# Performance work log

Measured on AMD Instinct MI355X. Metric: run time of the kernel, lower is better.

Reference implementation:

```python
import jax, jax.numpy as jnp
import numpy as np
import math

B, S, HID, H = 2, 1024, 768, 12
D = HID // H  # 64
ALPHA = 32.0


def setup_inputs() -> dict:
    key = jax.random.key(0)
    ks = jax.random.split(key, 8)
    return {
        "hidden_states": jax.random.normal(ks[0], (B, S, HID), jnp.float32),
        "attention_mask": jnp.zeros((B, 1, 1, S), jnp.float32),
        "head_mask": jnp.ones((1, H, 1, 1), jnp.float32),
        "rel_pos": jax.random.normal(ks[1], (B, H, S, S), jnp.float32),
        "rel_2d_pos": jax.random.normal(ks[2], (B, H, S, S), jnp.float32),
        "Wq": jax.random.normal(ks[3], (HID, HID), jnp.float32) * 0.02,
        "bq": jnp.zeros((HID,), jnp.float32),
        "Wk": jax.random.normal(ks[4], (HID, HID), jnp.float32) * 0.02,
        "bk": jnp.zeros((HID,), jnp.float32),
        "Wv": jax.random.normal(ks[5], (HID, HID), jnp.float32) * 0.02,
        "bv": jnp.zeros((HID,), jnp.float32),
    }


def _heads(x):
    # [B,S,HID] -> [B,H,S,D]
    return x.reshape(B, S, H, D).transpose(0, 2, 1, 3)


def cogview_softmax(scores, alpha=ALPHA):
    s = scores / alpha
    m = jnp.max(s, axis=-1, keepdims=True)
    return jax.nn.softmax((s - m) * alpha, axis=-1)


def reference(hidden_states, attention_mask, head_mask, rel_pos, rel_2d_pos,
              Wq, bq, Wk, bk, Wv, bv):
    norm = math.sqrt(D)
    q = _heads(hidden_states @ Wq + bq) / norm   # [B,H,S,D]
    k = _heads(hidden_states @ Wk + bk)
    v = _heads(hidden_states @ Wv + bv)
    scores = jnp.einsum("bhsd,bhtd->bhst", q, k)
    scores = scores + (rel_pos + rel_2d_pos) / norm
    scores = scores + attention_mask
    probs = cogview_softmax(scores)              # [B,H,S,S]
    probs = probs * head_mask
    ctx = jnp.einsum("bhst,bhtd->bhsd", probs, v)
    ctx = ctx.transpose(0, 2, 1, 3).reshape(B, S, HID)
    return ctx
```

## Files before the change

### kernel.cpp

```cpp
#include <hip/hip_runtime.h>
#include <hip/hip_bf16.h>
#include <cstdint>

#define BB   2
#define SS   1024
#define HIDD 768
#define NH   12
#define DH   64
#define BH   (BB*NH)

typedef short bf16x8 __attribute__((ext_vector_type(8)));
typedef float f32x4  __attribute__((ext_vector_type(4)));

__device__ __forceinline__ unsigned short f2b(float x) {
    union { float f; uint32_t u; } v; v.f = x;
    uint32_t u = v.u;
    uint32_t r = (u + 0x7fffu + ((u >> 16) & 1u)) >> 16;
    return (unsigned short)r;
}

__device__ __forceinline__ void async16(const void* g, void* l) {
    __builtin_amdgcn_global_load_lds(
        (const __attribute__((address_space(1))) unsigned int*)g,
        (__attribute__((address_space(3))) unsigned int*)l,
        16, 0, 0);
}

__global__ void cvt_x(const float* __restrict__ x, unsigned short* __restrict__ xb) {
    int i = blockIdx.x * blockDim.x + threadIdx.x;
    float4 v = ((const float4*)x)[i];
    ushort4 o;
    o.x = f2b(v.x); o.y = f2b(v.y); o.z = f2b(v.z); o.w = f2b(v.w);
    ((ushort4*)xb)[i] = o;
}

__global__ void transpose_w(const float* __restrict__ Wq, const float* __restrict__ Wk,
                            const float* __restrict__ Wv, unsigned short* __restrict__ Wt) {
    __shared__ float tile[32][33];
    const int w = blockIdx.z;
    const float* W = (w == 0) ? Wq : (w == 1) ? Wk : Wv;
    const int tx = threadIdx.x & 31, ty = threadIdx.x >> 5;
    const int k0 = blockIdx.x * 32, n0 = blockIdx.y * 32;
    for (int p = 0; p < 4; ++p)
        tile[ty + p * 8][tx] = W[(k0 + ty + p * 8) * HIDD + n0 + tx];
    __syncthreads();
    for (int p = 0; p < 4; ++p) {
        int n = n0 + ty + p * 8;
        Wt[(w * HIDD + n) * HIDD + k0 + tx] = f2b(tile[tx][ty + p * 8]);
    }
}

__global__ __launch_bounds__(256) void qkv_gemm(
    const unsigned short* __restrict__ Xb, const unsigned short* __restrict__ Wt,
    const float* __restrict__ bq, const float* __restrict__ bk, const float* __restrict__ bv,
    unsigned short* __restrict__ Qh, unsigned short* __restrict__ Kh,
    unsigned short* __restrict__ VhT) {
    __shared__ __align__(16) unsigned short lA[128 * 32];
    __shared__ __align__(16) unsigned short lB[128 * 32];
    const int t = threadIdx.x;
    const int wave = t >> 6, lane = t & 63;
    const int l15 = lane & 15, quad = lane >> 4;
    const int m0 = blockIdx.x * 128;
    const int n0 = blockIdx.y * 128;
    const int wm = (wave >> 1) * 64, wn = (wave & 1) * 64;

    f32x4 acc[4][4] = {};

    for (int k0 = 0; k0 < HIDD; k0 += 32) {
        __syncthreads();
        for (int r = 0; r < 2; ++r) {
            int i = r * 256 + t;
            int ldsbase = (r * 256 + wave * 64) * 8;
            async16(Xb + (m0 + (i >> 2)) * HIDD + k0 + (i & 3) * 8, &lA[ldsbase]);
            async16(Wt + (n0 + (i >> 2)) * HIDD + k0 + (i & 3) * 8, &lB[ldsbase]);
        }
        __syncthreads();

        bf16x8 af[4], bf[4];
        #pragma unroll
        for (int i = 0; i < 4; ++i)
            af[i] = *(const bf16x8*)&lA[(wm + i * 16 + l15) * 32 + quad * 8];
        #pragma unroll
        for (int j = 0; j < 4; ++j)
            bf[j] = *(const bf16x8*)&lB[(wn + j * 16 + l15) * 32 + quad * 8];
        #pragma unroll
        for (int i = 0; i < 4; ++i)
            #pragma unroll
            for (int j = 0; j < 4; ++j)
                acc[i][j] = __builtin_amdgcn_mfma_f32_16x16x32_bf16(af[i], bf[j], acc[i][j], 0, 0, 0);
    }

    const int sect = (n0 >= 1536) ? 2 : (n0 >= 768) ? 1 : 0;
    const float* bias = (sect == 0) ? bq : (sect == 1) ? bk : bv;
    #pragma unroll
    for (int i = 0; i < 4; ++i) {
        #pragma unroll
        for (int j = 0; j < 4; ++j) {
            int n  = n0 + wn + j * 16 + l15;
            int nn = n - sect * HIDD;
            int h = nn >> 6, d = nn & 63;
            float bval = bias[nn];
            #pragma unroll
            for (int r = 0; r < 4; ++r) {
                int m = m0 + wm + i * 16 + quad * 4 + r;
                int b = m >> 10, s = m & 1023;
                float v = acc[i][j][r] + bval;
                if (sect == 0) {
                    Qh[((size_t)(b * NH + h) * SS + s) * DH + d] = f2b(v * 0.125f);
                } else if (sect == 1) {
                    Kh[((size_t)(b * NH + h) * SS + s) * DH + d] = f2b(v);
                } else {
                    VhT[((size_t)(b * NH + h) * DH + d) * SS + s] = f2b(v);
                }
            }
        }
    }
}

__global__ __launch_bounds__(256) void flash_attn(
    const unsigned short* __restrict__ Qh, const unsigned short* __restrict__ Kh,
    const unsigned short* __restrict__ VhT,
    const float* __restrict__ rel, const float* __restrict__ rel2d,
    const float* __restrict__ amask, const float* __restrict__ hmask,
    float* __restrict__ out) {
    __shared__ __align__(16) unsigned short Plds[4][16 * 72];

    const int t = threadIdx.x;
    const int wave = t >> 6, lane = t & 63;
    const int l15 = lane & 15, quad = lane >> 4;
    const int bh = blockIdx.y;
    const int b = bh / NH, h = bh % NH;
    const int m0 = blockIdx.x * 64 + wave * 16;

    const unsigned short* Qp = Qh + (size_t)bh * SS * DH;
    const unsigned short* Kp = Kh + (size_t)bh * SS * DH;
    const unsigned short* Vp = VhT + (size_t)bh * DH * SS;
    const float* relp  = rel   + (size_t)bh * SS * SS;
    const float* rel2p = rel2d + (size_t)bh * SS * SS;
    const float* maskp = amask + (size_t)b * SS;

    bf16x8 qf0 = *(const bf16x8*)&Qp[(m0 + l15) * DH + quad * 8];
    bf16x8 qf1 = *(const bf16x8*)&Qp[(m0 + l15) * DH + 32 + quad * 8];

    f32x4 o[4] = {};
    float mrow[4] = {-1e30f, -1e30f, -1e30f, -1e30f};
    float lrow[4] = {0.f, 0.f, 0.f, 0.f};
    unsigned short* Pw = &Plds[wave][0];

    for (int j0 = 0; j0 < SS; j0 += 64) {
        f32x4 sc[4] = {};
        #pragma unroll
        for (int c = 0; c < 4; ++c) {
            bf16x8 k0f = *(const bf16x8*)&Kp[(j0 + c * 16 + l15) * DH + quad * 8];
            bf16x8 k1f = *(const bf16x8*)&Kp[(j0 + c * 16 + l15) * DH + 32 + quad * 8];
            sc[c] = __builtin_amdgcn_mfma_f32_16x16x32_bf16(qf0, k0f, sc[c], 0, 0, 0);
            sc[c] = __builtin_amdgcn_mfma_f32_16x16x32_bf16(qf1, k1f, sc[c], 0, 0, 0);
        }
        float sv[4][4];
        #pragma unroll
        for (int c = 0; c < 4; ++c) {
            int col = j0 + c * 16 + l15;
            float mk = maskp[col];
            #pragma unroll
            for (int r = 0; r < 4; ++r) {
                size_t idx = (size_t)(m0 + quad * 4 + r) * SS + col;
                sv[c][r] = sc[c][r] + (relp[idx] + rel2p[idx]) * 0.125f + mk;
            }
        }
        float alpha[4];
        #pragma unroll
        for (int r = 0; r < 4; ++r) {
            float mx = fmaxf(fmaxf(sv[0][r], sv[1][r]), fmaxf(sv[2][r], sv[3][r]));
            #pragma unroll
            for (int off = 1; off < 16; off <<= 1) mx = fmaxf(mx, __shfl_xor(mx, off, 64));
            float mnew = fmaxf(mrow[r], mx);
            alpha[r] = __expf(mrow[r] - mnew);
            mrow[r] = mnew;
            float rs = 0.f;
            #pragma unroll
            for (int c = 0; c < 4; ++c) {
                float p = __expf(sv[c][r] - mnew);
                sv[c][r] = p;
                rs += p;
            }
            #pragma unroll
            for (int off = 1; off < 16; off <<= 1) rs += __shfl_xor(rs, off, 64);
            lrow[r] = lrow[r] * alpha[r] + rs;
            o[0][r] *= alpha[r]; o[1][r] *= alpha[r]; o[2][r] *= alpha[r]; o[3][r] *= alpha[r];
        }
        #pragma unroll
        for (int c = 0; c < 4; ++c)
            #pragma unroll
            for (int r = 0; r < 4; ++r)
                Pw[(quad * 4 + r) * 72 + c * 16 + l15] = f2b(sv[c][r]);

        bf16x8 pf0 = *(const bf16x8*)&Pw[l15 * 72 + quad * 8];
        bf16x8 pf1 = *(const bf16x8*)&Pw[l15 * 72 + 32 + quad * 8];
        #pragma unroll
        for (int dt = 0; dt < 4; ++dt) {
            bf16x8 v0 = *(const bf16x8*)&Vp[(dt * 16 + l15) * SS + j0 + quad * 8];
            bf16x8 v1 = *(const bf16x8*)&Vp[(dt * 16 + l15) * SS + j0 + 32 + quad * 8];
            o[dt] = __builtin_amdgcn_mfma_f32_16x16x32_bf16(pf0, v0, o[dt], 0, 0, 0);
            o[dt] = __builtin_amdgcn_mfma_f32_16x16x32_bf16(pf1, v1, o[dt], 0, 0, 0);
        }
    }

    const float hm = hmask[h];
    #pragma unroll
    for (int r = 0; r < 4; ++r) {
        float inv = hm / lrow[r];
        int s = m0 + quad * 4 + r;
        float* op = out + ((size_t)(b * SS + s)) * HIDD + h * DH;
        #pragma unroll
        for (int dt = 0; dt < 4; ++dt) op[dt * 16 + l15] = o[dt][r] * inv;
    }
}

extern "C" void kernel_launch(void* const* d_in, const int* in_sizes, int n_in,
                              void* d_out, int out_size, void* d_ws, size_t ws_size,
                              hipStream_t stream) {
    const float* hs    = (const float*)d_in[0];
    const float* am    = (const float*)d_in[1];
    const float* hm    = (const float*)d_in[2];
    const float* rel   = (const float*)d_in[3];
    const float* rel2d = (const float*)d_in[4];
    const float* Wq    = (const float*)d_in[5];
    const float* bq    = (const float*)d_in[6];
    const float* Wk    = (const float*)d_in[7];
    const float* bk    = (const float*)d_in[8];
    const float* Wv    = (const float*)d_in[9];
    const float* bv    = (const float*)d_in[10];
    float* out = (float*)d_out;

    unsigned short* Xb  = (unsigned short*)d_ws;
    unsigned short* Wt  = Xb + 2048 * HIDD;
    unsigned short* Qh  = Wt + 3 * HIDD * HIDD;
    unsigned short* Kh  = Qh + (size_t)BH * SS * DH;
    unsigned short* VhT = Kh + (size_t)BH * SS * DH;

    cvt_x<<<(2048 * HIDD / 4) / 256, 256, 0, stream>>>(hs, Xb);
    dim3 gT(24, 24, 3);
    transpose_w<<<gT, 256, 0, stream>>>(Wq, Wk, Wv, Wt);
    dim3 gG(16, 18);
    qkv_gemm<<<gG, 256, 0, stream>>>(Xb, Wt, bq, bk, bv, Qh, Kh, VhT);
    dim3 gF(16, BH);
    flash_attn<<<gF, 256, 0, stream>>>(Qh, Kh, VhT, rel, rel2d, am, hm, out);
}
```

Before: 305.7 us.

## Split attention KV range across waves, shrink GEMM tile, add V transpose

Flash attention now gives each block 16 query rows and has its four waves each process a quarter of the key range, merging partial max/sum/output through shared memory. This quadruples the grid so more blocks are in flight while streaming the large rel_pos tensors. The QKV GEMM uses 64-row tiles, doubling its grid, and writes V in row layout with a coalesced store; a separate transpose kernel then builds V^T. The cost is an extra launch, an extra V round trip through memory, and an LDS reduction step in attention.

```diff
diff --git a/kernel.cpp b/kernel.cpp
--- a/kernel.cpp
+++ b/kernel.cpp
@@ -54,37 +54,40 @@
     const unsigned short* __restrict__ Xb, const unsigned short* __restrict__ Wt,
     const float* __restrict__ bq, const float* __restrict__ bk, const float* __restrict__ bv,
     unsigned short* __restrict__ Qh, unsigned short* __restrict__ Kh,
-    unsigned short* __restrict__ VhT) {
-    __shared__ __align__(16) unsigned short lA[128 * 32];
+    unsigned short* __restrict__ Vh) {
+    __shared__ __align__(16) unsigned short lA[64 * 32];
     __shared__ __align__(16) unsigned short lB[128 * 32];
     const int t = threadIdx.x;
     const int wave = t >> 6, lane = t & 63;
     const int l15 = lane & 15, quad = lane >> 4;
-    const int m0 = blockIdx.x * 128;
+    const int m0 = blockIdx.x * 64;
     const int n0 = blockIdx.y * 128;
-    const int wm = (wave >> 1) * 64, wn = (wave & 1) * 64;
-
-    f32x4 acc[4][4] = {};
+    const int wm = (wave >> 1) * 32, wn = (wave & 1) * 64;
+
+    f32x4 acc[2][4] = {};
 
     for (int k0 = 0; k0 < HIDD; k0 += 32) {
         __syncthreads();
-        for (int r = 0; r < 2; ++r) {
-            int i = r * 256 + t;
-            int ldsbase = (r * 256 + wave * 64) * 8;
-            async16(Xb + (m0 + (i >> 2)) * HIDD + k0 + (i & 3) * 8, &lA[ldsbase]);
-            async16(Wt + (n0 + (i >> 2)) * HIDD + k0 + (i & 3) * 8, &lB[ldsbase]);
+        {
+            int ldsA = (wave * 64) * 8;
+            async16(Xb + (m0 + (t >> 2)) * HIDD + k0 + (t & 3) * 8, &lA[ldsA]);
+            for (int r = 0; r < 2; ++r) {
+                int i = r * 256 + t;
+                int ldsB = (r * 256 + wave * 64) * 8;
+                async16(Wt + (n0 + (i >> 2)) * HIDD + k0 + (i & 3) * 8, &lB[ldsB]);
+            }
         }
         __syncthreads();
 
-        bf16x8 af[4], bf[4];
-        #pragma unroll
-        for (int i = 0; i < 4; ++i)
+        bf16x8 af[2], bf[4];
+        #pragma unroll
+        for (int i = 0; i < 2; ++i)
             af[i] = *(const bf16x8*)&lA[(wm + i * 16 + l15) * 32 + quad * 8];
         #pragma unroll
         for (int j = 0; j < 4; ++j)
             bf[j] = *(const bf16x8*)&lB[(wn + j * 16 + l15) * 32 + quad * 8];
         #pragma unroll
-        for (int i = 0; i < 4; ++i)
+        for (int i = 0; i < 2; ++i)
             #pragma unroll
             for (int j = 0; j < 4; ++j)
                 acc[i][j] = __builtin_amdgcn_mfma_f32_16x16x32_bf16(af[i], bf[j], acc[i][j], 0, 0, 0);
@@ -92,8 +95,10 @@
 
     const int sect = (n0 >= 1536) ? 2 : (n0 >= 768) ? 1 : 0;
     const float* bias = (sect == 0) ? bq : (sect == 1) ? bk : bv;
-    #pragma unroll
-    for (int i = 0; i < 4; ++i) {
+    unsigned short* dst = (sect == 0) ? Qh : (sect == 1) ? Kh : Vh;
+    const float scale = (sect == 0) ? 0.125f : 1.0f;
+    #pragma unroll
+    for (int i = 0; i < 2; ++i) {
         #pragma unroll
         for (int j = 0; j < 4; ++j) {
             int n  = n0 + wn + j * 16 + l15;
@@ -104,17 +109,29 @@
             for (int r = 0; r < 4; ++r) {
                 int m = m0 + wm + i * 16 + quad * 4 + r;
                 int b = m >> 10, s = m & 1023;
-                float v = acc[i][j][r] + bval;
-                if (sect == 0) {
-                    Qh[((size_t)(b * NH + h) * SS + s) * DH + d] = f2b(v * 0.125f);
-                } else if (sect == 1) {
-                    Kh[((size_t)(b * NH + h) * SS + s) * DH + d] = f2b(v);
-                } else {
-                    VhT[((size_t)(b * NH + h) * DH + d) * SS + s] = f2b(v);
-                }
-            }
-        }
-    }
+                float v = (acc[i][j][r] + bval) * scale;
+                dst[((size_t)(b * NH + h) * SS + s) * DH + d] = f2b(v);
+            }
+        }
+    }
+}
+
+__global__ __launch_bounds__(256) void transpose_v(
+    const unsigned short* __restrict__ Vh, unsigned short* __restrict__ VhT) {
+    __shared__ unsigned short tile[64][65];
+    const int t = threadIdx.x;
+    const int bh = blockIdx.y;
+    const int s0 = blockIdx.x * 64;
+    const int tx = t & 63, ty = t >> 6;
+    const unsigned short* src = Vh + (size_t)bh * SS * DH;
+    #pragma unroll
+    for (int p = 0; p < 16; ++p)
+        tile[ty + p * 4][tx] = src[(size_t)(s0 + ty + p * 4) * DH + tx];
+    __syncthreads();
+    unsigned short* dst = VhT + (size_t)bh * DH * SS;
+    #pragma unroll
+    for (int p = 0; p < 16; ++p)
+        dst[(size_t)(ty + p * 4) * SS + s0 + tx] = tile[tx][ty + p * 4];
 }
 
 __global__ __launch_bounds__(256) void flash_attn(
@@ -124,13 +141,16 @@
     const float* __restrict__ amask, const float* __restrict__ hmask,
     float* __restrict__ out) {
     __shared__ __align__(16) unsigned short Plds[4][16 * 72];
+    __shared__ float o_lds[4][16][64];
+    __shared__ float m_lds[4][16];
+    __shared__ float l_lds[4][16];
 
     const int t = threadIdx.x;
     const int wave = t >> 6, lane = t & 63;
     const int l15 = lane & 15, quad = lane >> 4;
     const int bh = blockIdx.y;
     const int b = bh / NH, h = bh % NH;
-    const int m0 = blockIdx.x * 64 + wave * 16;
+    const int m0 = blockIdx.x * 16;
 
     const unsigned short* Qp = Qh + (size_t)bh * SS * DH;
     const unsigned short* Kp = Kh + (size_t)bh * SS * DH;
@@ -147,7 +167,8 @@
     float lrow[4] = {0.f, 0.f, 0.f, 0.f};
     unsigned short* Pw = &Plds[wave][0];
 
-    for (int j0 = 0; j0 < SS; j0 += 64) {
+    const int jbeg = wave * 256, jend = jbeg + 256;
+    for (int j0 = jbeg; j0 < jend; j0 += 64) {
         f32x4 sc[4] = {};
         #pragma unroll
         for (int c = 0; c < 4; ++c) {
@@ -205,14 +226,37 @@
         }
     }
 
+    #pragma unroll
+    for (int dt = 0; dt < 4; ++dt)
+        #pragma unroll
+        for (int r = 0; r < 4; ++r)
+            o_lds[wave][quad * 4 + r][dt * 16 + l15] = o[dt][r];
+    if (l15 == 0) {
+        #pragma unroll
+        for (int r = 0; r < 4; ++r) {
+            m_lds[wave][quad * 4 + r] = mrow[r];
+            l_lds[wave][quad * 4 + r] = lrow[r];
+        }
+    }
+    __syncthreads();
+
     const float hm = hmask[h];
-    #pragma unroll
-    for (int r = 0; r < 4; ++r) {
-        float inv = hm / lrow[r];
-        int s = m0 + quad * 4 + r;
-        float* op = out + ((size_t)(b * SS + s)) * HIDD + h * DH;
-        #pragma unroll
-        for (int dt = 0; dt < 4; ++dt) op[dt * 16 + l15] = o[dt][r] * inv;
+    const int col = t & 63, rsel = t >> 6;
+    #pragma unroll
+    for (int rr = 0; rr < 4; ++rr) {
+        int row = rsel * 4 + rr;
+        float m01 = fmaxf(m_lds[0][row], m_lds[1][row]);
+        float m23 = fmaxf(m_lds[2][row], m_lds[3][row]);
+        float mt = fmaxf(m01, m23);
+        float lt = 0.f, val = 0.f;
+        #pragma unroll
+        for (int w = 0; w < 4; ++w) {
+            float sc = __expf(m_lds[w][row] - mt);
+            lt += sc * l_lds[w][row];
+            val += sc * o_lds[w][row][col];
+        }
+        int s = m0 + row;
+        out[((size_t)(b * SS + s)) * HIDD + h * DH + col] = val * hm / lt;
     }
 }
 
@@ -236,13 +280,16 @@
     unsigned short* Wt  = Xb + 2048 * HIDD;
     unsigned short* Qh  = Wt + 3 * HIDD * HIDD;
     unsigned short* Kh  = Qh + (size_t)BH * SS * DH;
-    unsigned short* VhT = Kh + (size_t)BH * SS * DH;
+    unsigned short* Vh  = Kh + (size_t)BH * SS * DH;
+    unsigned short* VhT = Vh + (size_t)BH * SS * DH;
 
     cvt_x<<<(2048 * HIDD / 4) / 256, 256, 0, stream>>>(hs, Xb);
     dim3 gT(24, 24, 3);
     transpose_w<<<gT, 256, 0, stream>>>(Wq, Wk, Wv, Wt);
-    dim3 gG(16, 18);
-    qkv_gemm<<<gG, 256, 0, stream>>>(Xb, Wt, bq, bk, bv, Qh, Kh, VhT);
-    dim3 gF(16, BH);
+    dim3 gG(32, 18);
+    qkv_gemm<<<gG, 256, 0, stream>>>(Xb, Wt, bq, bk, bv, Qh, Kh, Vh);
+    dim3 gV(16, BH);
+    transpose_v<<<gV, 256, 0, stream>>>(Vh, VhT);
+    dim3 gF(64, BH);
     flash_attn<<<gF, 256, 0, stream>>>(Qh, Kh, VhT, rel, rel2d, am, hm, out);
 }
```

Result: faster. 287.1 us (-6.1%).
